# Optimization experiments

Measured on AMD Instinct MI355X. Metric: run time of the kernel, lower is better.

Reference implementation:

```python
import jax, jax.numpy as jnp
import numpy as np

B, T, D, H = 2048, 32, 128, 128  # batch, time steps, input_size, hidden_size


def setup_inputs() -> dict:
    key = jax.random.key(0)
    ks = jax.random.split(key, 7)
    s = 1.0 / np.sqrt(H)  # pytorch default uniform init bound
    return {
        "input_data": jax.random.normal(ks[0], (B, T - 1, D), jnp.float32),
        "W_ih": jax.random.uniform(ks[1], (4 * H, D), jnp.float32, -s, s),
        "W_hh": jax.random.uniform(ks[2], (4 * H, H), jnp.float32, -s, s),
        "b_ih": jax.random.uniform(ks[3], (4 * H,), jnp.float32, -s, s),
        "b_hh": jax.random.uniform(ks[4], (4 * H,), jnp.float32, -s, s),
        "attn_w": jax.random.uniform(ks[5], (2 * H + T - 1,), jnp.float32, -s, s),
        "attn_b": jax.random.uniform(ks[6], (1,), jnp.float32, -s, s),
    }


def reference(input_data, W_ih, W_hh, b_ih, b_hh, attn_w, attn_b):
    Bb, Tm1, Dd = input_data.shape
    Hh = W_hh.shape[1]
    # attn_linear weight acts on cat([h, c, x_series]); split it into the three parts
    w_h, w_c, w_x = attn_w[:Hh], attn_w[Hh:2 * Hh], attn_w[2 * Hh:]
    # contribution of the full per-feature time series (constant across steps): [B, D]
    x_score = jnp.einsum('btd,t->bd', input_data, w_x)

    def step(carry, x_t):
        h, c = carry  # [B, H] each
        # hidden/cell are repeated across the D input features -> scalar-per-batch shift
        score = (h @ w_h + c @ w_c + attn_b[0])[:, None] + x_score  # [B, D]
        attn = jax.nn.softmax(score, axis=1)
        wx = attn * x_t  # weighted input, [B, D]
        # single-layer LSTM cell, pytorch gate order i, f, g, o
        gates = wx @ W_ih.T + b_ih + h @ W_hh.T + b_hh  # [B, 4H]
        i_g, f_g, g_g, o_g = jnp.split(gates, 4, axis=1)
        c_new = jax.nn.sigmoid(f_g) * c + jax.nn.sigmoid(i_g) * jnp.tanh(g_g)
        h_new = jax.nn.sigmoid(o_g) * jnp.tanh(c_new)
        return (h_new, c_new), (wx, h_new)

    h0 = jnp.zeros((Bb, Hh), input_data.dtype)
    c0 = jnp.zeros((Bb, Hh), input_data.dtype)
    xs = jnp.swapaxes(input_data, 0, 1)  # [T-1, B, D]
    _, (weighted, encoded) = jax.lax.scan(step, (h0, c0), xs)
    input_weighted = jnp.swapaxes(weighted, 0, 1)  # [B, T-1, D]
    input_encoded = jnp.swapaxes(encoded, 0, 1)    # [B, T-1, H]
    return input_weighted, input_encoded
```

## Files before the change

### kernel.cpp

```cpp
#include <hip/hip_runtime.h>

#define B_   2048
#define T1_  31
#define D_   128
#define MB_  8

typedef __attribute__((ext_vector_type(8))) short bf16x8;
typedef __attribute__((ext_vector_type(4))) float f32x4;
typedef __attribute__((ext_vector_type(2))) float f32x2;

__device__ __forceinline__ unsigned cvt_pk_bf16(float lo, float hi) {
    unsigned r;
    asm("v_cvt_pk_bf16_f32 %0, %1, %2" : "=v"(r) : "v"(lo), "v"(hi));
    return r;
}
__device__ __forceinline__ unsigned short f2bf(float f) {
    union { float f; unsigned u; } v; v.f = f;
    unsigned r = v.u + 0x7fffu + ((v.u >> 16) & 1u);
    return (unsigned short)(r >> 16);
}
__device__ __forceinline__ float rcpf_(float x) { return __builtin_amdgcn_rcpf(x); }
__device__ __forceinline__ float sigf(float x)  { return rcpf_(1.0f + __expf(-x)); }
__device__ __forceinline__ float tanhf_(float x) {
    float ax = fabsf(x);
    float t  = 1.0f - 2.0f * rcpf_(__expf(2.0f * ax) + 1.0f);
    return copysignf(t, x);
}

#define BAR_LDS() asm volatile("s_waitcnt lgkmcnt(0)\n\ts_barrier" ::: "memory")

__global__ __launch_bounds__(512, 2) void enc_fused(
    const float* __restrict__ in,
    const float* __restrict__ Wih,
    const float* __restrict__ Whh,
    const float* __restrict__ bih,
    const float* __restrict__ bhh,
    const float* __restrict__ aw,
    float* __restrict__ outW,
    float* __restrict__ outE)
{
    const int tid  = threadIdx.x;
    const int lane = tid & 63;
    const int wv   = tid >> 6;
    const int b0   = blockIdx.x * MB_;
    const int l15  = lane & 15;
    const int lq   = lane >> 4;

    __shared__ __align__(16) char Xw[30 * MB_ * 256];
    __shared__ __align__(16) char Hs[2 * MB_ * 256];

    bf16x8 bw[4][8];
    #pragma unroll
    for (int s = 0; s < 4; ++s) {
        int n = s * 128 + wv * 16 + l15;
        #pragma unroll
        for (int kf = 0; kf < 8; ++kf) {
            int kb = kf * 32 + lq * 8;
            const float* wp = (kf < 4) ? (Wih + n * D_ + kb) : (Whh + n * D_ + (kb - 128));
            float4 fa = *(const float4*)(wp);
            float4 fb = *(const float4*)(wp + 4);
            union { bf16x8 v; unsigned u[4]; } tmp;
            tmp.u[0] = cvt_pk_bf16(fa.x, fa.y);
            tmp.u[1] = cvt_pk_bf16(fa.z, fa.w);
            tmp.u[2] = cvt_pk_bf16(fb.x, fb.y);
            tmp.u[3] = cvt_pk_bf16(fb.z, fb.w);
            bw[s][kf] = tmp.v;
        }
    }
    const int col = wv * 16 + l15;
    const float bs0 = bih[col]           + bhh[col];
    const float bs1 = bih[128 + col]     + bhh[128 + col];
    const float bs2 = bih[256 + col]     + bhh[256 + col];
    const float bs3 = bih[384 + col]     + bhh[384 + col];

    const int mg = wv;
    const int dh = lane;
    const int d0 = 2 * dh;
    const float* pin = in + (size_t)(b0 + mg) * (T1_ * D_) + d0;

    float2 xc[T1_];
    float xs0 = 0.f, xs1 = 0.f;
    #pragma unroll
    for (int t = 0; t < T1_; ++t) {
        float wt = aw[2 * D_ + t];
        xc[t] = *(const float2*)(pin + t * D_);
        xs0 = fmaf(wt, xc[t].x, xs0);
        xs1 = fmaf(wt, xc[t].y, xs1);
    }
    float* attnS = (float*)Xw;
    attnS[mg * 128 + d0]     = xs0;
    attnS[mg * 128 + d0 + 1] = xs1;

    float v0 = attnS[mg * 128 + lane];
    float v1 = attnS[mg * 128 + lane + 64];
    float mx = fmaxf(v0, v1);
    #pragma unroll
    for (int o = 32; o > 0; o >>= 1) mx = fmaxf(mx, __shfl_xor(mx, o));
    float e0 = __expf(v0 - mx), e1 = __expf(v1 - mx);
    float ss = e0 + e1;
    #pragma unroll
    for (int o = 32; o > 0; o >>= 1) ss += __shfl_xor(ss, o);
    float inv = 1.0f / ss;
    attnS[mg * 128 + lane]      = e0 * inv;
    attnS[mg * 128 + lane + 64] = e1 * inv;
    const float a0 = attnS[mg * 128 + d0];
    const float a1 = attnS[mg * 128 + d0 + 1];
    __syncthreads();

    const int wxbyte = (4 * dh) ^ (mg << 4);
    float* outWp = outW + (size_t)(b0 + mg) * (T1_ * D_) + d0;
    unsigned wx30 = 0;
    #pragma unroll
    for (int t = 0; t < T1_; ++t) {
        float w0 = a0 * xc[t].x, w1 = a1 * xc[t].y;
        f32x2 wsv; wsv[0] = w0; wsv[1] = w1;
        __builtin_nontemporal_store(wsv, (f32x2*)(outWp + t * D_));
        unsigned u = cvt_pk_bf16(w0, w1);
        if (t < 30) *(unsigned*)(Xw + t * 2048 + mg * 256 + wxbyte) = u;
        else        wx30 = u;
    }
    ((unsigned*)Hs)[tid]       = 0u;
    ((unsigned*)Hs)[tid + 512] = 0u;
    __syncthreads();

    const int arow = l15 & 7;
    const int asw  = arow << 4;
    bf16x8 wxfr[4];
    #pragma unroll
    for (int kf = 0; kf < 4; ++kf)
        wxfr[kf] = *(const bf16x8*)(Xw + arow * 256 + ((kf * 64 + lq * 16) ^ asw));

    const int rb = ((lane & 31) >> 4) * 4 + ((lane >> 5) << 1);
    const bool hi32 = (lane >= 32);
    float cs0 = 0.f, cs1 = 0.f;
    float* outE0 = outE + (size_t)(b0 + rb)     * (T1_ * D_) + col;
    float* outE1 = outE + (size_t)(b0 + rb + 1) * (T1_ * D_) + col;

    f32x4 accx[4];
    #pragma unroll
    for (int s = 0; s < 4; ++s) {
        f32x4 a_ = {0.f, 0.f, 0.f, 0.f};
        #pragma unroll
        for (int kf = 0; kf < 4; ++kf)
            a_ = __builtin_amdgcn_mfma_f32_16x16x32_bf16(wxfr[kf], bw[s][kf], a_, 0, 0, 0);
        accx[s] = a_;
    }

    for (int t = 0; t < T1_; ++t) {
        const char* hp = Hs + (t & 1) * 2048 + arow * 256;
        bf16x8 hfr[4];
        #pragma unroll
        for (int kf = 0; kf < 4; ++kf)
            hfr[kf] = *(const bf16x8*)(hp + ((kf * 64 + lq * 16) ^ asw));

        if (t == 1)
            *(unsigned*)(Xw + mg * 256 + wxbyte) = wx30;

        f32x4 acc[4];
        #pragma unroll
        for (int s = 0; s < 4; ++s) {
            f32x4 a_ = accx[s];
            #pragma unroll
            for (int kf = 0; kf < 4; ++kf)
                a_ = __builtin_amdgcn_mfma_f32_16x16x32_bf16(hfr[kf], bw[s][4 + kf], a_, 0, 0, 0);
            acc[s] = a_;
        }

        if (t < 30) {
            int slot = (t + 1 == 30) ? 0 : (t + 1);
            #pragma unroll
            for (int kf = 0; kf < 4; ++kf)
                wxfr[kf] = *(const bf16x8*)(Xw + slot * 2048 + arow * 256 + ((kf * 64 + lq * 16) ^ asw));
        }

        float gq0[4], gq1[4];
        #pragma unroll
        for (int s = 0; s < 4; ++s) {
            gq0[s] = hi32 ? acc[s][2] : acc[s][0];
            gq1[s] = hi32 ? acc[s][3] : acc[s][1];
        }

        float iv, fv, gv, ov, cn, hh;
        iv = gq0[0] + bs0; fv = gq0[1] + bs1; gv = gq0[2] + bs2; ov = gq0[3] + bs3;
        cn = sigf(fv) * cs0 + sigf(iv) * tanhf_(gv); cs0 = cn;
        hh = sigf(ov) * tanhf_(cn);
        __builtin_nontemporal_store(hh, outE0 + t * D_);
        unsigned short hb0 = f2bf(hh);

        iv = gq1[0] + bs0; fv = gq1[1] + bs1; gv = gq1[2] + bs2; ov = gq1[3] + bs3;
        cn = sigf(fv) * cs1 + sigf(iv) * tanhf_(gv); cs1 = cn;
        hh = sigf(ov) * tanhf_(cn);
        __builtin_nontemporal_store(hh, outE1 + t * D_);
        unsigned short hb1 = f2bf(hh);

        if (t < 30) {
            char* hw = Hs + ((t + 1) & 1) * 2048;
            *(unsigned short*)(hw + rb * 256       + ((2 * col) ^ (rb << 4)))       = hb0;
            *(unsigned short*)(hw + (rb + 1) * 256 + ((2 * col) ^ ((rb + 1) << 4))) = hb1;

            #pragma unroll
            for (int s = 0; s < 4; ++s) {
                f32x4 a_ = {0.f, 0.f, 0.f, 0.f};
                #pragma unroll
                for (int kf = 0; kf < 4; ++kf)
                    a_ = __builtin_amdgcn_mfma_f32_16x16x32_bf16(wxfr[kf], bw[s][kf], a_, 0, 0, 0);
                accx[s] = a_;
            }
        }
        BAR_LDS();
    }
}

extern "C" void kernel_launch(void* const* d_in, const int* in_sizes, int n_in,
                              void* d_out, int out_size, void* d_ws, size_t ws_size,
                              hipStream_t stream) {
    const float* in  = (const float*)d_in[0];
    const float* Wih = (const float*)d_in[1];
    const float* Whh = (const float*)d_in[2];
    const float* bih = (const float*)d_in[3];
    const float* bhh = (const float*)d_in[4];
    const float* aw  = (const float*)d_in[5];

    float* outW = (float*)d_out;
    float* outE = outW + (size_t)B_ * T1_ * D_;

    enc_fused<<<dim3(B_ / MB_), dim3(512), 0, stream>>>(in, Wih, Whh, bih, bhh, aw, outW, outE);
}
```

Baseline: 55.59 us.

## Compute input projection in-loop and split recurrent MFMA chains into two accumulators

Moves the Wx·W_ih MFMA block from the tail of the previous iteration to the start of each step, ahead of the recurrent MFMAs. The h·W_hh product is split into two independent accumulator chains that are then summed, which shortens the dependent MFMA chain on the critical path. The global stores of h are moved after the LDS writes of the next hidden state, so the shared-memory handoff is issued before the stores. In exchange, the input projection now sits in the per-step critical section before the barrier rather than overlapping the previous step's tail, which may lengthen each step.

```diff
diff --git a/kernel.cpp b/kernel.cpp
--- a/kernel.cpp
+++ b/kernel.cpp
@@ -136,16 +136,6 @@
     float* outE0 = outE + (size_t)(b0 + rb)     * (T1_ * D_) + col;
     float* outE1 = outE + (size_t)(b0 + rb + 1) * (T1_ * D_) + col;
 
-    f32x4 accx[4];
-    #pragma unroll
-    for (int s = 0; s < 4; ++s) {
-        f32x4 a_ = {0.f, 0.f, 0.f, 0.f};
-        #pragma unroll
-        for (int kf = 0; kf < 4; ++kf)
-            a_ = __builtin_amdgcn_mfma_f32_16x16x32_bf16(wxfr[kf], bw[s][kf], a_, 0, 0, 0);
-        accx[s] = a_;
-    }
-
     for (int t = 0; t < T1_; ++t) {
         const char* hp = Hs + (t & 1) * 2048 + arow * 256;
         bf16x8 hfr[4];
@@ -156,14 +146,26 @@
         if (t == 1)
             *(unsigned*)(Xw + mg * 256 + wxbyte) = wx30;
 
-        f32x4 acc[4];
+        f32x4 accx[4];
         #pragma unroll
         for (int s = 0; s < 4; ++s) {
-            f32x4 a_ = accx[s];
+            f32x4 a_ = {0.f, 0.f, 0.f, 0.f};
             #pragma unroll
             for (int kf = 0; kf < 4; ++kf)
-                a_ = __builtin_amdgcn_mfma_f32_16x16x32_bf16(hfr[kf], bw[s][4 + kf], a_, 0, 0, 0);
-            acc[s] = a_;
+                a_ = __builtin_amdgcn_mfma_f32_16x16x32_bf16(wxfr[kf], bw[s][kf], a_, 0, 0, 0);
+            accx[s] = a_;
+        }
+
+        f32x4 acc[4];
+        #pragma unroll
+        for (int s = 0; s < 4; ++s) {
+            f32x4 zA = {0.f, 0.f, 0.f, 0.f};
+            f32x4 zB = {0.f, 0.f, 0.f, 0.f};
+            zA = __builtin_amdgcn_mfma_f32_16x16x32_bf16(hfr[0], bw[s][4], zA, 0, 0, 0);
+            zB = __builtin_amdgcn_mfma_f32_16x16x32_bf16(hfr[2], bw[s][6], zB, 0, 0, 0);
+            zA = __builtin_amdgcn_mfma_f32_16x16x32_bf16(hfr[1], bw[s][5], zA, 0, 0, 0);
+            zB = __builtin_amdgcn_mfma_f32_16x16x32_bf16(hfr[3], bw[s][7], zB, 0, 0, 0);
+            acc[s] = accx[s] + zA + zB;
         }
 
         if (t < 30) {
@@ -180,33 +182,25 @@
             gq1[s] = hi32 ? acc[s][3] : acc[s][1];
         }
 
-        float iv, fv, gv, ov, cn, hh;
+        float iv, fv, gv, ov, cn, hh0, hh1;
         iv = gq0[0] + bs0; fv = gq0[1] + bs1; gv = gq0[2] + bs2; ov = gq0[3] + bs3;
         cn = sigf(fv) * cs0 + sigf(iv) * tanhf_(gv); cs0 = cn;
-        hh = sigf(ov) * tanhf_(cn);
-        __builtin_nontemporal_store(hh, outE0 + t * D_);
-        unsigned short hb0 = f2bf(hh);
+        hh0 = sigf(ov) * tanhf_(cn);
+        unsigned short hb0 = f2bf(hh0);
 
         iv = gq1[0] + bs0; fv = gq1[1] + bs1; gv = gq1[2] + bs2; ov = gq1[3] + bs3;
         cn = sigf(fv) * cs1 + sigf(iv) * tanhf_(gv); cs1 = cn;
-        hh = sigf(ov) * tanhf_(cn);
-        __builtin_nontemporal_store(hh, outE1 + t * D_);
-        unsigned short hb1 = f2bf(hh);
+        hh1 = sigf(ov) * tanhf_(cn);
+        unsigned short hb1 = f2bf(hh1);
 
         if (t < 30) {
             char* hw = Hs + ((t + 1) & 1) * 2048;
             *(unsigned short*)(hw + rb * 256       + ((2 * col) ^ (rb << 4)))       = hb0;
             *(unsigned short*)(hw + (rb + 1) * 256 + ((2 * col) ^ ((rb + 1) << 4))) = hb1;
-
-            #pragma unroll
-            for (int s = 0; s < 4; ++s) {
-                f32x4 a_ = {0.f, 0.f, 0.f, 0.f};
-                #pragma unroll
-                for (int kf = 0; kf < 4; ++kf)
-                    a_ = __builtin_amdgcn_mfma_f32_16x16x32_bf16(wxfr[kf], bw[s][kf], a_, 0, 0, 0);
-                accx[s] = a_;
-            }
-        }
+        }
+        __builtin_nontemporal_store(hh0, outE0 + t * D_);
+        __builtin_nontemporal_store(hh1, outE1 + t * D_);
+
         BAR_LDS();
     }
 }
```

Result: slower. 58.69 us (+5.6%).
